# Performance work log

Hardware: AMD Instinct MI355X
Metric: run time of the kernel (lower is better)

The kernel has to match this reference:

```python
import jax, jax.numpy as jnp
import numpy as np
import math

L_MAX = 8  # matches init_kwargs max_angular
N_PAIR = 1_000_000


def setup_inputs() -> dict:
    key = jax.random.key(0)
    R = jax.random.normal(key, (N_PAIR, 3), dtype=jnp.float32)
    return {"R": R}


def _solid_harmonics(R, l_max):
    """Real solid harmonics r^l * Y_l^m (Wikipedia convention, sphericart math).

    Returns a tuple of arrays, one per l, each of shape [N, 2l+1], with m
    ordered -l..l (sin terms, m=0, cos terms).
    """
    x, y, z = R[:, 0], R[:, 1], R[:, 2]
    r2 = x * x + y * y + z * z
    one = jnp.ones_like(x)

    # c_m + i s_m = (x + i y)^m  ->  c_m = r_xy^m cos(m phi), s_m = r_xy^m sin(m phi)
    c = [one]
    s = [jnp.zeros_like(x)]
    for m in range(1, l_max + 1):
        c.append(x * c[m - 1] - y * s[m - 1])
        s.append(x * s[m - 1] + y * c[m - 1])

    # Q_l^m(z, r): r^{l-m} * (associated-Legendre part), via degree recurrence.
    # Q_l^l = -(2l-1) Q_{l-1}^{l-1};  Q_l^{l-1} = (2l-1) z Q_{l-1}^{l-1};
    # Q_l^m = ((2l-1) z Q_{l-1}^m - (l+m-1) r^2 Q_{l-2}^m) / (l-m)
    Q = {(0, 0): one}
    for l in range(1, l_max + 1):
        Q[(l, l)] = -(2 * l - 1) * Q[(l - 1, l - 1)]
        Q[(l, l - 1)] = (2 * l - 1) * z * Q[(l - 1, l - 1)]
        for m in range(l - 2, -1, -1):
            Q[(l, m)] = ((2 * l - 1) * z * Q[(l - 1, m)]
                         - (l + m - 1) * r2 * Q[(l - 2, m)]) / (l - m)

    def F(l, m):
        # (-1)^m cancels the Condon-Shortley phase inside Q -> Wikipedia convention
        return ((-1.0) ** m) * math.sqrt(
            (2 * l + 1) / (2 * math.pi)
            * math.factorial(l - m) / math.factorial(l + m))

    out = []
    for l in range(l_max + 1):
        cols = []
        for m in range(l, 0, -1):           # m = -l .. -1 (sin branch)
            cols.append(F(l, m) * Q[(l, m)] * s[m])
        cols.append(math.sqrt((2 * l + 1) / (4 * math.pi)) * Q[(l, 0)])  # m = 0
        for m in range(1, l + 1):           # m = 1 .. l (cos branch)
            cols.append(F(l, m) * Q[(l, m)] * c[m])
        out.append(jnp.stack(cols, axis=-1))  # [N, 2l+1]
    return tuple(out)


def reference(R):
    # Mirrors SolidHarmonics.forward: expansion split per degree l.
    return _solid_harmonics(R, L_MAX)
```

## Files before the change

### kernel.cpp

```cpp
#include <hip/hip_runtime.h>
#include <math.h>
#include <stdint.h>

#define LMAX 8
#define NPB 256

struct Coefs {
    float F[LMAX + 1][LMAX + 1];
    float A[LMAX + 1][LMAX + 1];
    float B[LMAX + 1][LMAX + 1];
};

__global__ __launch_bounds__(256) void solid_harmonics_kernel(
    const float* __restrict__ R, float* __restrict__ out, int N, Coefs cf)
{
    __shared__ __align__(16) float tile[NPB * (2 * LMAX + 1)];

    const int t = threadIdx.x;
    const int i0 = blockIdx.x * NPB;
    const int i = i0 + t;
    const int rows = min(NPB, N - i0);
    const bool valid = (i < N);

    float x = 0.f, y = 0.f, z = 0.f;
    if (valid) {
        x = R[3 * i + 0];
        y = R[3 * i + 1];
        z = R[3 * i + 2];
    }
    const float r2 = x * x + y * y + z * z;

    float c[LMAX + 1], s[LMAX + 1];
    c[0] = 1.f; s[0] = 0.f;

    float Qcur[LMAX + 1], Qm1[LMAX + 1], Qm2[LMAX + 1];
    Qcur[0] = 1.f;

#pragma unroll
    for (int l = 0; l <= LMAX; ++l) {
        if (l >= 1) {
#pragma unroll
            for (int m = 0; m < l - 1; ++m) Qm2[m] = Qm1[m];
#pragma unroll
            for (int m = 0; m < l; ++m) Qm1[m] = Qcur[m];
            c[l] = x * c[l - 1] - y * s[l - 1];
            s[l] = x * s[l - 1] + y * c[l - 1];
            Qcur[l]     = -(2.f * l - 1.f) * Qm1[l - 1];
            Qcur[l - 1] =  (2.f * l - 1.f) * z * Qm1[l - 1];
#pragma unroll
            for (int m = l - 2; m >= 0; --m)
                Qcur[m] = cf.A[l][m] * z * Qm1[m] - cf.B[l][m] * r2 * Qm2[m];
        }

        const int stride = 2 * l + 1;

        {
            float* row = &tile[t * stride];
#pragma unroll
            for (int m = l; m >= 1; --m) row[l - m] = cf.F[l][m] * Qcur[m] * s[m];
            row[l] = cf.F[l][0] * Qcur[0];
#pragma unroll
            for (int m = 1; m <= l; ++m) row[l + m] = cf.F[l][m] * Qcur[m] * c[m];
        }
        __syncthreads();

        {
            float* obase = out + (size_t)N * (size_t)(l * l) + (size_t)i0 * (size_t)stride;
            const int E = rows * stride;
            if ((((uintptr_t)obase) & 15u) == 0) {
                const int E4 = E >> 2;
                const float4* t4 = (const float4*)tile;
                float4* o4 = (float4*)obase;
                for (int e = t; e < E4; e += NPB) o4[e] = t4[e];
                for (int e = (E4 << 2) + t; e < E; e += NPB) obase[e] = tile[e];
            } else {
                for (int e = t; e < E; e += NPB) obase[e] = tile[e];
            }
        }
        __syncthreads();
    }
}

extern "C" void kernel_launch(void* const* d_in, const int* in_sizes, int n_in,
                              void* d_out, int out_size, void* d_ws, size_t ws_size,
                              hipStream_t stream) {
    const float* R = (const float*)d_in[0];
    float* out = (float*)d_out;
    const int N = in_sizes[0] / 3;

    Coefs cf;
    double fact[2 * LMAX + 1];
    fact[0] = 1.0;
    for (int k = 1; k <= 2 * LMAX; ++k) fact[k] = fact[k - 1] * (double)k;
    const double PI = 3.14159265358979323846;
    for (int l = 0; l <= LMAX; ++l) {
        for (int m = 0; m <= LMAX; ++m) { cf.F[l][m] = 0.f; cf.A[l][m] = 0.f; cf.B[l][m] = 0.f; }
        cf.F[l][0] = (float)sqrt((2.0 * l + 1.0) / (4.0 * PI));
        for (int m = 1; m <= l; ++m) {
            double sign = (m & 1) ? -1.0 : 1.0;
            cf.F[l][m] = (float)(sign * sqrt((2.0 * l + 1.0) / (2.0 * PI)
                                             * fact[l - m] / fact[l + m]));
        }
        for (int m = 0; m <= l - 2; ++m) {
            cf.A[l][m] = (float)((2.0 * l - 1.0) / (double)(l - m));
            cf.B[l][m] = (float)((double)(l + m - 1) / (double)(l - m));
        }
    }

    const int block = NPB;
    const int grid = (N + block - 1) / block;
    solid_harmonics_kernel<<<grid, block, 0, stream>>>(R, out, N, cf);
}
```

Measured before the change: 328.4 us.

## Stage all degrees in shared memory and flush once after a single barrier

Each thread now writes every degree's harmonics into one shared tile of 81 columns, with each degree stored as its own contiguous sub-block. A single __syncthreads is followed by the coalesced float4 copy-out for all degrees. This replaces the earlier per-degree pattern of compute, barrier, store, barrier. The goal is to remove the 18 barriers and let global stores issue back to back. To keep shared memory per block reasonable, the block size drops to 128, which raises LDS use per block to about 41 KB and may limit how many blocks fit on a CU.

```diff
diff --git a/kernel.cpp b/kernel.cpp
--- a/kernel.cpp
+++ b/kernel.cpp
@@ -3,7 +3,8 @@
 #include <stdint.h>
 
 #define LMAX 8
-#define NPB 256
+#define NPB 128
+#define NCOLS 81
 
 struct Coefs {
     float F[LMAX + 1][LMAX + 1];
@@ -11,19 +12,18 @@
     float B[LMAX + 1][LMAX + 1];
 };
 
-__global__ __launch_bounds__(256) void solid_harmonics_kernel(
+__global__ __launch_bounds__(NPB) void solid_harmonics_kernel(
     const float* __restrict__ R, float* __restrict__ out, int N, Coefs cf)
 {
-    __shared__ __align__(16) float tile[NPB * (2 * LMAX + 1)];
+    __shared__ __align__(16) float tile[NPB * NCOLS];
 
     const int t = threadIdx.x;
     const int i0 = blockIdx.x * NPB;
     const int i = i0 + t;
     const int rows = min(NPB, N - i0);
-    const bool valid = (i < N);
 
     float x = 0.f, y = 0.f, z = 0.f;
-    if (valid) {
+    if (i < N) {
         x = R[3 * i + 0];
         y = R[3 * i + 1];
         z = R[3 * i + 2];
@@ -51,33 +51,30 @@
             for (int m = l - 2; m >= 0; --m)
                 Qcur[m] = cf.A[l][m] * z * Qm1[m] - cf.B[l][m] * r2 * Qm2[m];
         }
+        float* row = &tile[NPB * l * l + t * (2 * l + 1)];
+#pragma unroll
+        for (int m = l; m >= 1; --m) row[l - m] = cf.F[l][m] * Qcur[m] * s[m];
+        row[l] = cf.F[l][0] * Qcur[0];
+#pragma unroll
+        for (int m = 1; m <= l; ++m) row[l + m] = cf.F[l][m] * Qcur[m] * c[m];
+    }
 
+    __syncthreads();
+
+#pragma unroll
+    for (int l = 0; l <= LMAX; ++l) {
         const int stride = 2 * l + 1;
-
-        {
-            float* row = &tile[t * stride];
-#pragma unroll
-            for (int m = l; m >= 1; --m) row[l - m] = cf.F[l][m] * Qcur[m] * s[m];
-            row[l] = cf.F[l][0] * Qcur[0];
-#pragma unroll
-            for (int m = 1; m <= l; ++m) row[l + m] = cf.F[l][m] * Qcur[m] * c[m];
+        const float* src = &tile[NPB * l * l];
+        float* obase = out + (size_t)N * (size_t)(l * l) + (size_t)i0 * (size_t)stride;
+        const int E = rows * stride;
+        if (((((uintptr_t)obase) & 15u) == 0) && rows == NPB) {
+            const int E4 = E >> 2;
+            const float4* s4 = (const float4*)src;
+            float4* o4 = (float4*)obase;
+            for (int e = t; e < E4; e += NPB) o4[e] = s4[e];
+        } else {
+            for (int e = t; e < E; e += NPB) obase[e] = src[e];
         }
-        __syncthreads();
-
-        {
-            float* obase = out + (size_t)N * (size_t)(l * l) + (size_t)i0 * (size_t)stride;
-            const int E = rows * stride;
-            if ((((uintptr_t)obase) & 15u) == 0) {
-                const int E4 = E >> 2;
-                const float4* t4 = (const float4*)tile;
-                float4* o4 = (float4*)obase;
-                for (int e = t; e < E4; e += NPB) o4[e] = t4[e];
-                for (int e = (E4 << 2) + t; e < E; e += NPB) obase[e] = tile[e];
-            } else {
-                for (int e = t; e < E; e += NPB) obase[e] = tile[e];
-            }
-        }
-        __syncthreads();
     }
 }
 
@@ -107,7 +104,6 @@
         }
     }
 
-    const int block = NPB;
-    const int grid = (N + block - 1) / block;
-    solid_harmonics_kernel<<<grid, block, 0, stream>>>(R, out, N, cf);
+    const int grid = (N + NPB - 1) / NPB;
+    solid_harmonics_kernel<<<grid, NPB, 0, stream>>>(R, out, N, cf);
 }
```

Measured after the change: 327.4 us. Within noise of the previous version (-0.3%).
